# Kernel optimization log

Measured on AMD Instinct MI355X. Metric: run time of the kernel, lower is better.

The kernel has to match this reference:

```python
import jax, jax.numpy as jnp
import numpy as np

NUM_HEADS = 16
N_EMBD = 1024
HEAD_SIZE = N_EMBD // NUM_HEADS
BLOCK_SIZE = 2048
B, T = 4, 2048


def setup_inputs() -> dict:
    key = jax.random.key(0)
    ks = jax.random.split(key, 6)
    x = jax.random.normal(ks[0], (B, T, N_EMBD), dtype=jnp.float32)
    s = 1.0 / np.sqrt(N_EMBD)
    # per-head q/k/v projections (bias=False), stacked over heads: [H, D, hs]
    Wq = jax.random.uniform(ks[1], (NUM_HEADS, N_EMBD, HEAD_SIZE), minval=-s, maxval=s, dtype=jnp.float32)
    Wk = jax.random.uniform(ks[2], (NUM_HEADS, N_EMBD, HEAD_SIZE), minval=-s, maxval=s, dtype=jnp.float32)
    Wv = jax.random.uniform(ks[3], (NUM_HEADS, N_EMBD, HEAD_SIZE), minval=-s, maxval=s, dtype=jnp.float32)
    # output projection nn.Linear(n_embd, n_embd): weight [D, D] (out, in) + bias [D]
    Wo = jax.random.uniform(ks[4], (N_EMBD, N_EMBD), minval=-s, maxval=s, dtype=jnp.float32)
    bo = jax.random.uniform(ks[5], (N_EMBD,), minval=-s, maxval=s, dtype=jnp.float32)
    return {"x": x, "Wq": Wq, "Wk": Wk, "Wv": Wv, "Wo": Wo, "bo": bo}


def _mha(x, Wq, Wk, Wv, Wo, bo):
    # project all heads at once: [B,T,D] x [H,D,hs] -> [B,H,T,hs]
    q = jnp.einsum("btd,hds->bhts", x, Wq)
    k = jnp.einsum("btd,hds->bhts", x, Wk)
    v = jnp.einsum("btd,hds->bhts", x, Wv)
    scale = jnp.asarray(HEAD_SIZE, x.dtype) ** -0.5
    scores = jnp.einsum("bhqs,bhks->bhqk", q, k) * scale  # [B,H,T,T]
    T_ = x.shape[1]
    causal = jnp.tril(jnp.ones((T_, T_), dtype=bool))
    scores = jnp.where(causal[None, None], scores, jnp.asarray(-jnp.inf, x.dtype))
    att = jax.nn.softmax(scores, axis=-1)
    out = jnp.einsum("bhqk,bhks->bhqs", att, v)  # [B,H,T,hs]
    # concat heads along last dim: [B,T,H*hs]
    out = out.transpose(0, 2, 1, 3).reshape(x.shape[0], T_, N_EMBD)
    # output projection (dropout=0.0 -> identity)
    return out @ Wo.T + bo


def reference(x, Wq, Wk, Wv, Wo, bo):
    return _mha(x, Wq, Wk, Wv, Wo, bo)
```

## Files before the change

kernel.cpp:

```cpp
#include <hip/hip_runtime.h>
#include <hip/hip_bf16.h>
#include <stdint.h>

typedef __bf16 bf16;
typedef __attribute__((ext_vector_type(8))) __bf16 bf16x8;
typedef __attribute__((ext_vector_type(4))) float f32x4;

#define NH     16
#define DM     1024
#define HS     64
#define BATCH  4
#define SEQ    2048
#define N_XE   (BATCH * SEQ * DM)
#define N_WOE  (DM * DM)

__device__ __forceinline__ void async16(void* lds, const void* g) {
  __builtin_amdgcn_global_load_lds(
      (const uint32_t __attribute__((address_space(1)))*)g,
      (uint32_t __attribute__((address_space(3)))*)lds,
      16, 0, 0);
}

__device__ __forceinline__ f32x4 mfma16(bf16x8 a, bf16x8 b, f32x4 c) {
  return __builtin_amdgcn_mfma_f32_16x16x32_bf16(a, b, c, 0, 0, 0);
}

__global__ void detect_mode(const unsigned short* __restrict__ x, int* flag) {
  int lane = threadIdx.x & 63;
  unsigned short v = x[2 * lane];
  int e = (v >> 7) & 0xFF;
  int sane = (e >= 90 && e <= 160) ? 1 : 0;
  #pragma unroll
  for (int s = 1; s < 64; s <<= 1) sane += __shfl_xor(sane, s, 64);
  if (threadIdx.x == 0) *flag = (sane >= 48) ? 0 : 1;
}

__global__ __launch_bounds__(256)
void convert_in(const void* __restrict__ x, const void* __restrict__ Wo,
                bf16* __restrict__ xb, bf16* __restrict__ Wob,
                const int* __restrict__ flagp) {
  const int f32m = *flagp;
  size_t base = ((size_t)blockIdx.x * 256 + threadIdx.x) * 8;
  const void* src; bf16* dst; size_t off;
  if (base < (size_t)N_XE) { src = x;  dst = xb;  off = base; }
  else                     { src = Wo; dst = Wob; off = base - N_XE; }
  if (f32m) {
    const float* s = (const float*)src + off;
    float4 a = *(const float4*)s;
    float4 b = *(const float4*)(s + 4);
    bf16x8 o;
    o[0] = (bf16)a.x; o[1] = (bf16)a.y; o[2] = (bf16)a.z; o[3] = (bf16)a.w;
    o[4] = (bf16)b.x; o[5] = (bf16)b.y; o[6] = (bf16)b.z; o[7] = (bf16)b.w;
    *(bf16x8*)(dst + off) = o;
  } else {
    *(bf16x8*)(dst + off) = *(const bf16x8*)((const bf16*)src + off);
  }
}

__global__ __launch_bounds__(256)
void transpose_w(const void* __restrict__ Wq, const void* __restrict__ Wk,
                 const void* __restrict__ Wv, bf16* __restrict__ WT,
                 const int* __restrict__ flagp) {
  __shared__ bf16 Ts[64][72];
  const int f32m = *flagp;
  const void* W = (blockIdx.y == 0) ? Wq : (blockIdx.y == 1) ? Wk : Wv;
  bf16* dst = WT + (size_t)blockIdx.y * DM * DM;
  const int h  = blockIdx.x >> 4;
  const int d0 = (blockIdx.x & 15) * 64;
  const int tid = threadIdx.x;
  #pragma unroll
  for (int p = 0; p < 2; ++p) {
    int idx = p * 256 + tid;
    int dr = idx >> 3, c = idx & 7;
    size_t eoff = (size_t)(h * DM + d0 + dr) * HS + c * 8;
    bf16x8 v;
    if (f32m) {
      const float* s = (const float*)W + eoff;
      #pragma unroll
      for (int j = 0; j < 8; ++j) v[j] = (bf16)s[j];
    } else {
      v = *(const bf16x8*)((const bf16*)W + eoff);
    }
    #pragma unroll
    for (int j = 0; j < 8; ++j) Ts[c * 8 + j][dr] = v[j];
  }
  __syncthreads();
  #pragma unroll
  for (int p = 0; p < 2; ++p) {
    int idx = p * 256 + tid;
    int sr = idx >> 3, c = idx & 7;
    bf16x8 v = *(const bf16x8*)(&Ts[sr][c * 8]);
    *(bf16x8*)(dst + (size_t)(h * 64 + sr) * DM + d0 + c * 8) = v;
  }
}

template<typename EpiF>
__device__ __forceinline__ void gemm128_bt(const bf16* __restrict__ A,
                                           const bf16* __restrict__ BT,
                                           int m0, int n0, EpiF epi) {
  __shared__ bf16 As[2][128 * 32];
  __shared__ bf16 Bs[2][128 * 32];
  const int tid  = threadIdx.x;
  const int wave = tid >> 6, lane = tid & 63;
  const int wr = wave >> 1, wc = wave & 1;
  const int fr = lane & 15, fg = lane >> 4;
  const int srow = lane >> 2;
  const int scb  = (lane & 3) * 16;
  f32x4 acc[4][4] = {};

  auto STAGE = [&](int buf, int k0) {
    #pragma unroll
    for (int i = 0; i < 2; ++i) {
      int chunk = wave * 2 + i;
      int row = chunk * 16 + srow;
      async16((char*)&As[buf][0] + chunk * 1024,
              (const char*)(A + (size_t)(m0 + row) * DM + k0) + scb);
      async16((char*)&Bs[buf][0] + chunk * 1024,
              (const char*)(BT + (size_t)(n0 + row) * DM + k0) + scb);
    }
  };

  STAGE(0, 0);
  #pragma unroll 1
  for (int t = 0; t < 32; ++t) {
    const int buf = t & 1;
    if (t + 1 < 32) {
      STAGE(buf ^ 1, (t + 1) * 32);
      asm volatile("s_waitcnt vmcnt(4)" ::: "memory");
    } else {
      asm volatile("s_waitcnt vmcnt(0)" ::: "memory");
    }
    __builtin_amdgcn_s_barrier();
    bf16x8 af[4], bv[4];
    #pragma unroll
    for (int mi = 0; mi < 4; ++mi)
      af[mi] = *(const bf16x8*)(&As[buf][(wr * 64 + mi * 16 + fr) * 32 + fg * 8]);
    #pragma unroll
    for (int ni = 0; ni < 4; ++ni)
      bv[ni] = *(const bf16x8*)(&Bs[buf][(wc * 64 + ni * 16 + fr) * 32 + fg * 8]);
    #pragma unroll
    for (int mi = 0; mi < 4; ++mi)
      #pragma unroll
      for (int ni = 0; ni < 4; ++ni)
        acc[mi][ni] = mfma16(af[mi], bv[ni], acc[mi][ni]);
    __builtin_amdgcn_s_barrier();
  }
  #pragma unroll
  for (int mi = 0; mi < 4; ++mi)
    #pragma unroll
    for (int ni = 0; ni < 4; ++ni)
      #pragma unroll
      for (int r = 0; r < 4; ++r) {
        int m = m0 + wr * 64 + mi * 16 + fg * 4 + r;
        int n = n0 + wc * 64 + ni * 16 + fr;
        epi(m, n, acc[mi][ni][r]);
      }
}

__global__ __launch_bounds__(256, 4)
void qkv_gemm(const bf16* __restrict__ x, const bf16* __restrict__ WT,
              bf16* __restrict__ Qb, bf16* __restrict__ Kb, bf16* __restrict__ Vt) {
  const int bid = blockIdx.x;
  const int m0 = (bid & 63) * 128;
  const int nz = bid >> 6;
  const int z  = nz >> 3;
  const int n0 = (nz & 7) * 128;
  const bf16* BT = WT + (size_t)z * DM * DM;
  gemm128_bt(x, BT, m0, n0, [&](int m, int n, float v) {
    int b = m >> 11, t = m & 2047, h = n >> 6, s = n & 63;
    if (z == 0)
      Qb[((size_t)(b * NH + h) * SEQ + t) * HS + s] = (bf16)v;
    else if (z == 1)
      Kb[((size_t)(b * NH + h) * SEQ + t) * HS + s] = (bf16)v;
    else
      Vt[((size_t)(b * NH + h) * HS + s) * SEQ + t] = (bf16)v;
  });
}

__global__ __launch_bounds__(256, 4)
void out_gemm(const bf16* __restrict__ att, const bf16* __restrict__ Wob,
              const void* __restrict__ bo, void* __restrict__ out,
              const int* __restrict__ flagp) {
  const int f32m = *flagp;
  const int bid = blockIdx.x;
  const int m0 = (bid & 63) * 128;
  const int n0 = (bid >> 6) * 128;
  gemm128_bt(att, Wob, m0, n0, [&](int m, int n, float v) {
    float bv = f32m ? ((const float*)bo)[n] : (float)((const bf16*)bo)[n];
    float o = v + bv;
    if (f32m) ((float*)out)[(size_t)m * DM + n] = o;
    else      ((bf16*)out)[(size_t)m * DM + n] = (bf16)o;
  });
}

#define KVB  64
__global__ __launch_bounds__(256, 2)
void attn_kernel(const bf16* __restrict__ Qb, const bf16* __restrict__ Kb,
                 const bf16* __restrict__ Vt, bf16* __restrict__ att) {
  __shared__ bf16 Ks[2][64][64];
  __shared__ bf16 Vs[2][64][64];
  __shared__ bf16 Ps[4][2][16][64];
  const int wave = threadIdx.x >> 6, lane = threadIdx.x & 63;
  const int fr = lane & 15, fg = lane >> 4;
  const int pair = blockIdx.x;
  const int bh = blockIdx.y;
  const bf16* Qp = Qb + (size_t)bh * SEQ * HS;
  const bf16* Kp = Kb + (size_t)bh * SEQ * HS;
  const bf16* Vp = Vt + (size_t)bh * HS * SEQ;
  const int b = bh >> 4, h = bh & 15;

  const int srow8 = lane >> 3;
  const int schk  = (lane & 7) ^ srow8;

  #pragma unroll
  for (int seg = 0; seg < 2; ++seg) {
    const int qb = seg == 0 ? (15 - pair) : pair;
    const int q0 = qb * 128 + wave * 32;
    const int kv_hi = q0 + 32;
    const int nt = (qb + 1) * 2;

    bf16x8 qf[2][2];
    #pragma unroll
    for (int qt = 0; qt < 2; ++qt)
      #pragma unroll
      for (int hh = 0; hh < 2; ++hh)
        qf[qt][hh] = *(const bf16x8*)(Qp + (size_t)(q0 + qt * 16 + fr) * HS + hh * 32 + fg * 8);

    float rs[2][4] = {};
    f32x4 accO[2][4] = {};

    auto STAGE = [&](int buf, int kvb) {
      #pragma unroll
      for (int i = 0; i < 2; ++i) {
        int r8 = wave * 16 + i * 8;
        async16(&Ks[buf][r8][0], Kp + (size_t)(kvb + r8 + srow8) * HS + schk * 8);
        async16(&Vs[buf][r8][0], Vp + (size_t)(r8 + srow8) * SEQ + kvb + schk * 8);
      }
    };

    STAGE(0, 0);
    for (int t = 0; t < nt; ++t) {
      const int buf = t & 1;
      const int kvb = t * KVB;
      if (t + 1 < nt) {
        STAGE(buf ^ 1, kvb + KVB);
        asm volatile("s_waitcnt vmcnt(4)" ::: "memory");
      } else {
        asm volatile("s_waitcnt vmcnt(0)" ::: "memory");
      }
      __builtin_amdgcn_s_barrier();
      if (kvb < kv_hi) {
        bf16x8 kf[4][2];
        #pragma unroll
        for (int s = 0; s < 4; ++s)
          #pragma unroll
          for (int hh = 0; hh < 2; ++hh)
            kf[s][hh] = *(const bf16x8*)(&Ks[buf][s * 16 + fr][((hh * 4 + fg) ^ (fr & 7)) * 8]);
        asm volatile("s_waitcnt lgkmcnt(0)" ::: "memory");

        #pragma unroll
        for (int qt = 0; qt < 2; ++qt) {
          f32x4 sc[4];
          #pragma unroll
          for (int s = 0; s < 4; ++s) {
            sc[s] = f32x4{0.f, 0.f, 0.f, 0.f};
            sc[s] = mfma16(qf[qt][0], kf[s][0], sc[s]);
            sc[s] = mfma16(qf[qt][1], kf[s][1], sc[s]);
          }
          #pragma unroll
          for (int s = 0; s < 4; ++s)
            #pragma unroll
            for (int r = 0; r < 4; ++r) {
              int qrow = q0 + qt * 16 + fg * 4 + r;
              int col  = kvb + s * 16 + fr;
              float p = __expf(sc[s][r] * 0.125f);
              p = (col <= qrow) ? p : 0.f;
              rs[qt][r] += p;
              int row = fg * 4 + r;
              int swz = (s * 2 + (fr >> 3)) ^ (row & 7);
              Ps[wave][qt][row][swz * 8 + (fr & 7)] = (bf16)p;
            }
        }
        asm volatile("s_waitcnt lgkmcnt(0)" ::: "memory");
        __builtin_amdgcn_sched_barrier(0);
        bf16x8 pf[2][2];
        #pragma unroll
        for (int qt = 0; qt < 2; ++qt)
          #pragma unroll
          for (int kc = 0; kc < 2; ++kc)
            pf[qt][kc] = *(const bf16x8*)(&Ps[wave][qt][fr][(((kc * 4 + fg) ^ (fr & 7))) * 8]);
        #pragma unroll
        for (int st = 0; st < 4; ++st) {
          bf16x8 vf0 = *(const bf16x8*)(&Vs[buf][st * 16 + fr][((fg) ^ (fr & 7)) * 8]);
          bf16x8 vf1 = *(const bf16x8*)(&Vs[buf][st * 16 + fr][((4 + fg) ^ (fr & 7)) * 8]);
          #pragma unroll
          for (int qt = 0; qt < 2; ++qt) {
            accO[qt][st] = mfma16(pf[qt][0], vf0, accO[qt][st]);
            accO[qt][st] = mfma16(pf[qt][1], vf1, accO[qt][st]);
          }
        }
      }
      __builtin_amdgcn_s_barrier();
    }

    #pragma unroll
    for (int sh = 1; sh < 16; sh <<= 1)
      #pragma unroll
      for (int qt = 0; qt < 2; ++qt)
        #pragma unroll
        for (int r = 0; r < 4; ++r)
          rs[qt][r] += __shfl_xor(rs[qt][r], sh, 64);
    #pragma unroll
    for (int qt = 0; qt < 2; ++qt)
      #pragma unroll
      for (int st = 0; st < 4; ++st)
        #pragma unroll
        for (int r = 0; r < 4; ++r) {
          int qrow = q0 + qt * 16 + fg * 4 + r;
          float o = accO[qt][st][r] / rs[qt][r];
          att[((size_t)(b * SEQ + qrow)) * DM + h * 64 + st * 16 + fr] = (bf16)o;
        }
  }
}

extern "C" void kernel_launch(void* const* d_in, const int* in_sizes, int n_in,
                              void* d_out, int out_size, void* d_ws, size_t ws_size,
                              hipStream_t stream) {
  const void* x  = d_in[0];
  const void* Wq = d_in[1];
  const void* Wk = d_in[2];
  const void* Wv = d_in[3];
  const void* Wo = d_in[4];
  const void* bo = d_in[5];

  char* ws = (char*)d_ws;
  int*  flag = (int*)ws;
  bf16* xb  = (bf16*)(ws + 256);
  bf16* WT  = (bf16*)(ws + 256 + ((size_t)16 << 20));
  bf16* Wob = (bf16*)(ws + 256 + ((size_t)22 << 20));
  bf16* Qb  = (bf16*)(ws + 256 + ((size_t)24 << 20));
  bf16* Kb  = (bf16*)(ws + 256 + ((size_t)40 << 20));
  bf16* Vt  = (bf16*)(ws + 256 + ((size_t)56 << 20));
  bf16* att = xb;

  detect_mode<<<1, 64, 0, stream>>>((const unsigned short*)x, flag);
  convert_in<<<(N_XE + N_WOE) / 2048, 256, 0, stream>>>(x, Wo, xb, Wob, flag);
  transpose_w<<<dim3(256, 3), 256, 0, stream>>>(Wq, Wk, Wv, WT, flag);
  qkv_gemm<<<dim3(1536), 256, 0, stream>>>(xb, WT, Qb, Kb, Vt);
  attn_kernel<<<dim3(8, BATCH * NH), 256, 0, stream>>>(Qb, Kb, Vt, att);
  out_gemm<<<dim3(512), 256, 0, stream>>>(att, Wob, bo, d_out, flag);
}
```

Baseline: 286.6 us.

## Replace 128x128 GEMM with 256x256 8-wave phased kernel with swizzled LDS

The QKV and output GEMMs move from a 128x128x32 tile with 4 waves to a 256x256x64 tile with 8 waves. The K loop is split into four phases that interleave async staging of the next tile with MFMA work, use s_setprio around the MFMAs, and use an XOR-swizzled LDS layout to avoid bank conflicts. Block indices are remapped so that tiles sharing rows land on the same XCD, aiming for better L2 reuse. The larger tiles cut global/LDS traffic per flop, but launch far fewer blocks (384 and 128), which may underfill the GPU, especially for out_gemm.

```diff
diff --git a/kernel.cpp b/kernel.cpp
--- a/kernel.cpp
+++ b/kernel.cpp
@@ -13,6 +13,7 @@
 #define SEQ    2048
 #define N_XE   (BATCH * SEQ * DM)
 #define N_WOE  (DM * DM)
+#define NKT    16
 
 __device__ __forceinline__ void async16(void* lds, const void* g) {
   __builtin_amdgcn_global_load_lds(
@@ -94,79 +95,119 @@
   }
 }
 
+__device__ __forceinline__ bf16x8 ldsfrag(const bf16* base, int r, int kk, int fg) {
+  return *(const bf16x8*)(base + r * 64 + (((kk * 4 + fg) ^ (r & 7)) * 8));
+}
+
 template<typename EpiF>
-__device__ __forceinline__ void gemm128_bt(const bf16* __restrict__ A,
-                                           const bf16* __restrict__ BT,
-                                           int m0, int n0, EpiF epi) {
-  __shared__ bf16 As[2][128 * 32];
-  __shared__ bf16 Bs[2][128 * 32];
+__device__ __forceinline__ void gemm256_8ph(const bf16* __restrict__ A,
+                                            const bf16* __restrict__ BT,
+                                            int m0, int n0, EpiF epi) {
+  __shared__ bf16 As[2][256 * 64];
+  __shared__ bf16 Bs[2][256 * 64];
   const int tid  = threadIdx.x;
-  const int wave = tid >> 6, lane = tid & 63;
-  const int wr = wave >> 1, wc = wave & 1;
+  const int wid  = tid >> 6, lane = tid & 63;
+  const int wr = wid >> 2, wc = wid & 3;
   const int fr = lane & 15, fg = lane >> 4;
-  const int srow = lane >> 2;
-  const int scb  = (lane & 3) * 16;
-  f32x4 acc[4][4] = {};
-
-  auto STAGE = [&](int buf, int k0) {
-    #pragma unroll
-    for (int i = 0; i < 2; ++i) {
-      int chunk = wave * 2 + i;
-      int row = chunk * 16 + srow;
-      async16((char*)&As[buf][0] + chunk * 1024,
-              (const char*)(A + (size_t)(m0 + row) * DM + k0) + scb);
-      async16((char*)&Bs[buf][0] + chunk * 1024,
-              (const char*)(BT + (size_t)(n0 + row) * DM + k0) + scb);
+  const int srow = tid >> 3;
+  const int scg  = (tid & 7) ^ (srow & 7);
+  f32x4 acc[8][4] = {};
+
+  auto STAGE_PART = [&](int buf, int kt, int j) {
+    async16((char*)&As[buf][0] + j * 8192 + wid * 1024,
+            A + (size_t)(m0 + j * 64 + srow) * DM + kt * 64 + scg * 8);
+    async16((char*)&Bs[buf][0] + j * 8192 + wid * 1024,
+            BT + (size_t)(n0 + j * 64 + srow) * DM + kt * 64 + scg * 8);
+  };
+
+  #pragma unroll
+  for (int j = 0; j < 4; ++j) STAGE_PART(0, 0, j);
+
+  bf16x8 af[8], bfr[8];
+  #pragma unroll 1
+  for (int kt = 0; kt < NKT; ++kt) {
+    const int buf = kt & 1;
+    const bool pre = (kt + 1) < NKT;
+    #pragma unroll
+    for (int q = 0; q < 4; ++q) {
+      if (q == 0) {
+        if (pre) {
+          STAGE_PART(buf ^ 1, kt + 1, 0);
+          asm volatile("s_waitcnt vmcnt(2)" ::: "memory");
+        } else {
+          asm volatile("s_waitcnt vmcnt(0)" ::: "memory");
+        }
+        __builtin_amdgcn_s_barrier();
+        asm volatile("" ::: "memory");
+        #pragma unroll
+        for (int i = 0; i < 4; ++i) {
+          int r = wr * 128 + i * 16 + fr;
+          #pragma unroll
+          for (int kk = 0; kk < 2; ++kk)
+            af[i * 2 + kk] = ldsfrag(&As[buf][0], r, kk, fg);
+        }
+        #pragma unroll
+        for (int i = 0; i < 4; ++i) {
+          int r = wc * 64 + i * 16 + fr;
+          #pragma unroll
+          for (int kk = 0; kk < 2; ++kk)
+            bfr[i * 2 + kk] = ldsfrag(&Bs[buf][0], r, kk, fg);
+        }
+      } else {
+        if (q == 2) {
+          #pragma unroll
+          for (int i = 0; i < 4; ++i) {
+            int r = wr * 128 + 64 + i * 16 + fr;
+            #pragma unroll
+            for (int kk = 0; kk < 2; ++kk)
+              af[i * 2 + kk] = ldsfrag(&As[buf][0], r, kk, fg);
+          }
+        }
+        if (pre) STAGE_PART(buf ^ 1, kt + 1, q);
+        __builtin_amdgcn_s_barrier();
+        asm volatile("" ::: "memory");
+      }
+      const int mio = (q >> 1) * 4, nio = (q & 1) * 2;
+      __builtin_amdgcn_s_setprio(1);
+      #pragma unroll
+      for (int i = 0; i < 4; ++i)
+        #pragma unroll
+        for (int nj = 0; nj < 2; ++nj)
+          #pragma unroll
+          for (int kk = 0; kk < 2; ++kk)
+            acc[mio + i][nio + nj] =
+                mfma16(af[i * 2 + kk], bfr[(nio + nj) * 2 + kk], acc[mio + i][nio + nj]);
+      __builtin_amdgcn_s_setprio(0);
+      __builtin_amdgcn_s_barrier();
+      asm volatile("" ::: "memory");
     }
-  };
-
-  STAGE(0, 0);
-  #pragma unroll 1
-  for (int t = 0; t < 32; ++t) {
-    const int buf = t & 1;
-    if (t + 1 < 32) {
-      STAGE(buf ^ 1, (t + 1) * 32);
-      asm volatile("s_waitcnt vmcnt(4)" ::: "memory");
-    } else {
-      asm volatile("s_waitcnt vmcnt(0)" ::: "memory");
-    }
-    __builtin_amdgcn_s_barrier();
-    bf16x8 af[4], bv[4];
-    #pragma unroll
-    for (int mi = 0; mi < 4; ++mi)
-      af[mi] = *(const bf16x8*)(&As[buf][(wr * 64 + mi * 16 + fr) * 32 + fg * 8]);
+  }
+  #pragma unroll
+  for (int mi = 0; mi < 8; ++mi)
     #pragma unroll
     for (int ni = 0; ni < 4; ++ni)
-      bv[ni] = *(const bf16x8*)(&Bs[buf][(wc * 64 + ni * 16 + fr) * 32 + fg * 8]);
-    #pragma unroll
-    for (int mi = 0; mi < 4; ++mi)
-      #pragma unroll
-      for (int ni = 0; ni < 4; ++ni)
-        acc[mi][ni] = mfma16(af[mi], bv[ni], acc[mi][ni]);
-    __builtin_amdgcn_s_barrier();
-  }
-  #pragma unroll
-  for (int mi = 0; mi < 4; ++mi)
-    #pragma unroll
-    for (int ni = 0; ni < 4; ++ni)
-      #pragma unroll
-      for (int r = 0; r < 4; ++r) {
-        int m = m0 + wr * 64 + mi * 16 + fg * 4 + r;
-        int n = n0 + wc * 64 + ni * 16 + fr;
-        epi(m, n, acc[mi][ni][r]);
-      }
-}
-
-__global__ __launch_bounds__(256, 4)
+      #pragma unroll
+      for (int rr = 0; rr < 4; ++rr) {
+        int m = m0 + wr * 128 + mi * 16 + fg * 4 + rr;
+        int n = wc * 64 + ni * 16 + fr;
+        epi(m, n, acc[mi][ni][rr]);
+      }
+}
+
+__global__ __launch_bounds__(512, 2)
 void qkv_gemm(const bf16* __restrict__ x, const bf16* __restrict__ WT,
               bf16* __restrict__ Qb, bf16* __restrict__ Kb, bf16* __restrict__ Vt) {
-  const int bid = blockIdx.x;
-  const int m0 = (bid & 63) * 128;
-  const int nz = bid >> 6;
-  const int z  = nz >> 3;
-  const int n0 = (nz & 7) * 128;
-  const bf16* BT = WT + (size_t)z * DM * DM;
-  gemm128_bt(x, BT, m0, n0, [&](int m, int n, float v) {
+  const int xcd = blockIdx.x & 7;
+  const int k   = blockIdx.x >> 3;
+  const int m_tile = xcd * 4 + k / 12;
+  const int nz = k % 12;
+  const int z  = nz >> 2;
+  const int n_tile = nz & 3;
+  const int m0 = m_tile * 256;
+  const int nb = n_tile * 256;
+  const bf16* BT = WT + (size_t)z * DM * DM + (size_t)nb * DM;
+  gemm256_8ph(x, BT, m0, 0, [&](int m, int nrel, float v) {
+    int n = nb + nrel;
     int b = m >> 11, t = m & 2047, h = n >> 6, s = n & 63;
     if (z == 0)
       Qb[((size_t)(b * NH + h) * SEQ + t) * HS + s] = (bf16)v;
@@ -177,15 +218,20 @@
   });
 }
 
-__global__ __launch_bounds__(256, 4)
+__global__ __launch_bounds__(512, 2)
 void out_gemm(const bf16* __restrict__ att, const bf16* __restrict__ Wob,
               const void* __restrict__ bo, void* __restrict__ out,
               const int* __restrict__ flagp) {
   const int f32m = *flagp;
-  const int bid = blockIdx.x;
-  const int m0 = (bid & 63) * 128;
-  const int n0 = (bid >> 6) * 128;
-  gemm128_bt(att, Wob, m0, n0, [&](int m, int n, float v) {
+  const int xcd = blockIdx.x & 7;
+  const int k   = blockIdx.x >> 3;
+  const int m_tile = xcd * 4 + (k >> 2);
+  const int n_tile = k & 3;
+  const int m0 = m_tile * 256;
+  const int nb = n_tile * 256;
+  const bf16* BT = Wob + (size_t)nb * DM;
+  gemm256_8ph(att, BT, m0, 0, [&](int m, int nrel, float v) {
+    int n = nb + nrel;
     float bv = f32m ? ((const float*)bo)[n] : (float)((const bf16*)bo)[n];
     float o = v + bv;
     if (f32m) ((float*)out)[(size_t)m * DM + n] = o;
@@ -346,7 +392,7 @@
   detect_mode<<<1, 64, 0, stream>>>((const unsigned short*)x, flag);
   convert_in<<<(N_XE + N_WOE) / 2048, 256, 0, stream>>>(x, Wo, xb, Wob, flag);
   transpose_w<<<dim3(256, 3), 256, 0, stream>>>(Wq, Wk, Wv, WT, flag);
-  qkv_gemm<<<dim3(1536), 256, 0, stream>>>(xb, WT, Qb, Kb, Vt);
+  qkv_gemm<<<dim3(384), 512, 0, stream>>>(xb, WT, Qb, Kb, Vt);
   attn_kernel<<<dim3(8, BATCH * NH), 256, 0, stream>>>(Qb, Kb, Vt, att);
-  out_gemm<<<dim3(512), 256, 0, stream>>>(att, Wob, bo, d_out, flag);
-}
+  out_gemm<<<dim3(128), 512, 0, stream>>>(att, Wob, bo, d_out, flag);
+}
```

Measured after the change: 320.8 us. +11.9%, slower.
